# Kernel optimization log

Hardware: AMD Instinct MI355X
Metric: run time of the kernel (lower is better)

The kernel has to match this reference:

```python
import jax, jax.numpy as jnp
import numpy as np

V_SZ = 32000  # vocab_tar_size
D = 256       # embed / lstm / attn units
B, T, S = 32, 64, 128

def setup_inputs() -> dict:
    key = jax.random.key(0)
    ks = jax.random.split(key, 16)
    sc = lambda *shape: 1.0 / np.sqrt(shape[0])
    inp = {
        "tokens": jax.random.randint(ks[0], (B, T), 0, V_SZ),
        "h0": jax.random.normal(ks[1], (B, D), jnp.float32),
        "c0": jax.random.normal(ks[2], (B, D), jnp.float32),
        "enc_out": jax.random.normal(ks[3], (B, S, D), jnp.float32),
        # embedding table
        "E": jax.random.normal(ks[4], (V_SZ, D), jnp.float32) * 0.02,
        # attention: W1 (query), W2 (values/keys), V (score)
        "Wq": jax.random.normal(ks[5], (D, D), jnp.float32) * sc(D),
        "bq": jnp.zeros((D,), jnp.float32),
        "Wk": jax.random.normal(ks[6], (D, D), jnp.float32) * sc(D),
        "bk": jnp.zeros((D,), jnp.float32),
        "Vw": jax.random.normal(ks[7], (D, 1), jnp.float32) * sc(D),
        "bv": jnp.zeros((1,), jnp.float32),
        # LSTM: input dim 2D (context||embed), gates i,f,g,o
        "Wx": jax.random.normal(ks[8], (2 * D, 4 * D), jnp.float32) * sc(2 * D),
        "Wh": jax.random.normal(ks[9], (D, 4 * D), jnp.float32) * sc(D),
        "b_lstm": jnp.zeros((4 * D,), jnp.float32),
        # output projection + softmax
        "Wo": jax.random.normal(ks[10], (D, V_SZ), jnp.float32) * sc(D),
        "bo": jnp.zeros((V_SZ,), jnp.float32),
    }
    return inp


def reference(tokens, h0, c0, enc_out, E, Wq, bq, Wk, bk, Vw, bv,
              Wx, Wh, b_lstm, Wo, bo):
    # Precompute W2(values): same math as per-step recompute. [B,S,D]
    keys = enc_out @ Wk + bk

    def step(carry, tok):
        h, c = carry
        emb = E[tok]                                   # [B,D]
        # Bahdanau attention, query = h
        q = h @ Wq + bq                                # [B,D]
        score = jnp.tanh(q[:, None, :] + keys) @ Vw + bv   # [B,S,1]
        attn = jax.nn.softmax(score, axis=1)           # softmax over S
        ctx = jnp.sum(attn * enc_out, axis=1)          # [B,D]
        x = jnp.concatenate([ctx, emb], axis=-1)       # [B,2D]
        z = x @ Wx + h @ Wh + b_lstm                   # [B,4D]
        i, f, g, o = jnp.split(z, 4, axis=-1)          # keras gate order i,f,c,o
        c_new = jax.nn.sigmoid(f) * c + jax.nn.sigmoid(i) * jnp.tanh(g)
        h_new = jax.nn.sigmoid(o) * jnp.tanh(c_new)
        probs = jax.nn.softmax(h_new @ Wo + bo, axis=-1)   # [B,V]
        return (h_new, c_new), probs

    (_, _), outs = jax.lax.scan(step, (h0, c0), tokens.T)  # outs: [T,B,V]
    return jnp.transpose(outs, (1, 0, 2))                  # [B,T,V]
```

## Files before the change

kernel.cpp:

```cpp
#include <hip/hip_runtime.h>

#define Bz 32
#define Tz 64
#define Sz 128
#define Dz 256
#define Vz 32000

__device__ __forceinline__ float sigmf(float x){ return 1.0f/(1.0f + __expf(-x)); }
__device__ __forceinline__ float tanhfast(float x){ float e = __expf(2.0f*x); return 1.0f - 2.0f/(e+1.0f); }

__global__ void k_keys(const float* __restrict__ enc, const float* __restrict__ Wk,
                       const float* __restrict__ bk, float* __restrict__ keys){
  const int blk = blockIdx.x;
  const int tid = threadIdx.x;
  const int b  = blk >> 3;
  const int s0 = (blk & 7) * 16;
  const float* ebase = enc + (b*Sz + s0)*Dz;
  const int d = tid;
  float acc[16];
  #pragma unroll
  for (int i = 0; i < 16; ++i) acc[i] = 0.f;
  for (int k = 0; k < Dz; k += 4){
    float w0 = Wk[(k+0)*Dz + d];
    float w1 = Wk[(k+1)*Dz + d];
    float w2 = Wk[(k+2)*Dz + d];
    float w3 = Wk[(k+3)*Dz + d];
    #pragma unroll
    for (int si = 0; si < 16; ++si){
      float4 ev = *(const float4*)(ebase + si*Dz + k);
      acc[si] += ev.x*w0 + ev.y*w1 + ev.z*w2 + ev.w*w3;
    }
  }
  const float bkd = bk[d];
  #pragma unroll
  for (int si = 0; si < 16; ++si)
    keys[(b*Sz + s0 + si)*Dz + d] = acc[si] + bkd;
}

__global__ void __launch_bounds__(256) k_encw(const float* __restrict__ enc,
                                              const float* __restrict__ Wx,
                                              float* __restrict__ encW,
                                              unsigned* flags){
  const int tid = threadIdx.x;
  if (blockIdx.x == 0) flags[tid] = 0u;
  const int row0 = blockIdx.x * 4;
  const int u4 = tid * 4;
  float4 a0 = {0,0,0,0}, a1 = {0,0,0,0}, a2 = {0,0,0,0}, a3 = {0,0,0,0};
  for (int d = 0; d < Dz; ++d){
    float4 wv = *(const float4*)(Wx + (size_t)d*1024 + u4);
    float e0 = enc[(size_t)(row0+0)*Dz + d];
    float e1 = enc[(size_t)(row0+1)*Dz + d];
    float e2 = enc[(size_t)(row0+2)*Dz + d];
    float e3 = enc[(size_t)(row0+3)*Dz + d];
    a0.x += e0*wv.x; a0.y += e0*wv.y; a0.z += e0*wv.z; a0.w += e0*wv.w;
    a1.x += e1*wv.x; a1.y += e1*wv.y; a1.z += e1*wv.z; a1.w += e1*wv.w;
    a2.x += e2*wv.x; a2.y += e2*wv.y; a2.z += e2*wv.z; a2.w += e2*wv.w;
    a3.x += e3*wv.x; a3.y += e3*wv.y; a3.z += e3*wv.z; a3.w += e3*wv.w;
  }
  *(float4*)(encW + (size_t)(row0+0)*1024 + u4) = a0;
  *(float4*)(encW + (size_t)(row0+1)*1024 + u4) = a1;
  *(float4*)(encW + (size_t)(row0+2)*1024 + u4) = a2;
  *(float4*)(encW + (size_t)(row0+3)*1024 + u4) = a3;
}

__global__ void __launch_bounds__(1024) k_recur(
    const int* __restrict__ tok, const float* __restrict__ h0, const float* __restrict__ c0,
    const float* __restrict__ Emb,
    const float* __restrict__ Wq, const float* __restrict__ bq,
    const float* __restrict__ Vw, const float* __restrict__ bv,
    const float* __restrict__ Wx, const float* __restrict__ Wh,
    const float* __restrict__ bl, const float* __restrict__ keys,
    const float* __restrict__ encW,
    float* __restrict__ hs, float* xch, unsigned* flags)
{
  const int tid = threadIdx.x;
  const int blk = blockIdx.x;
  const int b = ((blk >> 6) << 3) | (blk & 7);
  const int s = (blk >> 3) & 7;

  __shared__ float ew[Sz*128];
  __shared__ float xe[512];
  __shared__ float qv[Dz];
  __shared__ float vl[Dz];
  __shared__ float scp[Sz];
  __shared__ float selds[Sz+1];
  __shared__ float zp[1024];
  __shared__ float zl[128];
  __shared__ float hnl[32];
  __shared__ float clds[32];
  __shared__ float qpp[1024];

  const int u_local = tid & 127;
  const int kc = tid >> 7;
  const int u_gate = ((u_local >> 5) << 8) + (s << 5) + (u_local & 31);
  const int dq = tid & 255;
  const int jc = tid >> 8;

  float w[64];
  {
    const float* wbase = (kc < 4) ? (Wx + (size_t)(256 + kc*64)*1024 + u_gate)
                                  : (Wh + (size_t)((kc-4)*64)*1024 + u_gate);
    #pragma unroll
    for (int i = 0; i < 64; ++i) w[i] = wbase[(size_t)i*1024];
  }
  float wq[8];
  #pragma unroll
  for (int jj = 0; jj < 8; ++jj) wq[jj] = Wq[(size_t)(s*32 + jc*8 + jj)*Dz + dq];

  #pragma unroll
  for (int i = 0; i < 16; ++i){
    int idx = tid + i*1024;
    int srow = idx >> 7, ul = idx & 127;
    int ug = ((ul >> 5) << 8) + (s << 5) + (ul & 31);
    ew[idx] = encW[(size_t)(b*Sz + srow)*1024 + ug];
  }

  if (tid < Dz) vl[tid] = Vw[tid];
  if (tid < 32) clds[tid] = c0[b*Dz + s*32 + tid];

  {
    float qp = 0.f;
    #pragma unroll
    for (int jj = 0; jj < 8; ++jj) qp += h0[b*Dz + s*32 + jc*8 + jj] * wq[jj];
    qpp[jc*256 + dq] = qp;
  }
  __syncthreads();
  {
    float* x0 = xch + (size_t)((b*8) + s)*288;
    if (tid < 256)
      __hip_atomic_store(x0 + tid, qpp[tid] + qpp[256+tid] + qpp[512+tid] + qpp[768+tid],
                         __ATOMIC_RELAXED, __HIP_MEMORY_SCOPE_AGENT);
    else if (tid < 288)
      __hip_atomic_store(x0 + tid, h0[b*Dz + s*32 + (tid-256)],
                         __ATOMIC_RELAXED, __HIP_MEMORY_SCOPE_AGENT);
  }
  __syncthreads();
  if (tid == 0)
    __hip_atomic_store(flags + b*8 + s, 1u, __ATOMIC_RELAXED, __HIP_MEMORY_SCOPE_AGENT);

  const float bv0 = bv[0];
  const int ss = tid >> 3, p8 = tid & 7;

  for (int t = 0; t < Tz; ++t){
    if (tid < 64){
      const unsigned tgt = (unsigned)(t+1);
      while (__hip_atomic_load(flags + b*8 + (tid & 7), __ATOMIC_RELAXED, __HIP_MEMORY_SCOPE_AGENT) < tgt)
        __builtin_amdgcn_s_sleep(1);
      __builtin_amdgcn_fence(__ATOMIC_ACQUIRE, "workgroup");
    }
    __syncthreads();
    const float* xcp = xch + (size_t)((t & 1)*256 + b*8)*288;
    if (tid < 256){
      float q = bq[tid];
      #pragma unroll
      for (int s2 = 0; s2 < 8; ++s2)
        q += __hip_atomic_load(xcp + s2*288 + tid, __ATOMIC_RELAXED, __HIP_MEMORY_SCOPE_AGENT);
      qv[tid] = q;
    } else if (tid < 512){
      int u = tid - 256;
      xe[256 + u] = __hip_atomic_load(xcp + (u >> 5)*288 + 256 + (u & 31),
                                      __ATOMIC_RELAXED, __HIP_MEMORY_SCOPE_AGENT);
    } else if (tid < 768){
      int eidx = tid - 512;
      int tk = tok[b*Tz + t];
      xe[eidx] = Emb[(size_t)tk*Dz + eidx];
    }
    __syncthreads();
    {
      const float* kp = keys + (size_t)(b*Sz + ss)*Dz;
      float a = 0.f;
      #pragma unroll
      for (int j4 = 0; j4 < 8; ++j4){
        const int d0 = j4*32 + p8*4;
        float4 kv = *(const float4*)(kp + d0);
        float4 qj = *(const float4*)(qv + d0);
        float4 vj = *(const float4*)(vl + d0);
        a += tanhfast(qj.x + kv.x) * vj.x;
        a += tanhfast(qj.y + kv.y) * vj.y;
        a += tanhfast(qj.z + kv.z) * vj.z;
        a += tanhfast(qj.w + kv.w) * vj.w;
      }
      a += __shfl_down(a, 4);
      a += __shfl_down(a, 2);
      a += __shfl_down(a, 1);
      if (p8 == 0) scp[ss] = a;
    }
    __syncthreads();
    if (tid < Sz) selds[tid] = __expf(scp[tid] + bv0);
    __syncthreads();
    if (tid < 64){
      float v = selds[tid] + selds[tid+64];
      #pragma unroll
      for (int off = 32; off > 0; off >>= 1) v += __shfl_down(v, off);
      if (tid == 0) selds[Sz] = 1.0f / v;
    }
    __syncthreads();
    {
      float acc1 = 0.f;
      const float* xep = xe + kc*64;
      #pragma unroll
      for (int i4 = 0; i4 < 16; ++i4){
        float4 xv = *(const float4*)(xep + i4*4);
        acc1 += xv.x*w[i4*4+0] + xv.y*w[i4*4+1] + xv.z*w[i4*4+2] + xv.w*w[i4*4+3];
      }
      float acc2 = 0.f;
      const float* ewp = ew + kc*16*128 + u_local;
      #pragma unroll
      for (int m = 0; m < 16; ++m)
        acc2 = __builtin_fmaf(selds[kc*16 + m], ewp[m*128], acc2);
      zp[kc*128 + u_local] = acc1 + selds[Sz]*acc2;
    }
    __syncthreads();
    if (tid < 128){
      float z = bl[((tid >> 5) << 8) + s*32 + (tid & 31)];
      #pragma unroll
      for (int k2 = 0; k2 < 8; ++k2) z += zp[k2*128 + tid];
      zl[tid] = z;
    }
    __syncthreads();
    if (tid < 32){
      float zi = zl[tid], zf = zl[32+tid], zg = zl[64+tid], zo = zl[96+tid];
      float cn = sigmf(zf)*clds[tid] + sigmf(zi)*tanhfast(zg);
      float hn = sigmf(zo)*tanhfast(cn);
      clds[tid] = cn; hnl[tid] = hn;
      hs[(size_t)(t*Bz + b)*Dz + s*32 + tid] = hn;
    }
    __syncthreads();
    if (t < Tz-1){
      {
        float qp = 0.f;
        #pragma unroll
        for (int jj = 0; jj < 8; ++jj) qp += hnl[jc*8 + jj] * wq[jj];
        qpp[jc*256 + dq] = qp;
      }
      __syncthreads();
      {
        float* xn = xch + (size_t)(((t+1) & 1)*256 + b*8 + s)*288;
        if (tid < 256)
          __hip_atomic_store(xn + tid, qpp[tid] + qpp[256+tid] + qpp[512+tid] + qpp[768+tid],
                             __ATOMIC_RELAXED, __HIP_MEMORY_SCOPE_AGENT);
        else if (tid < 288)
          __hip_atomic_store(xn + tid, hnl[tid - 256],
                             __ATOMIC_RELAXED, __HIP_MEMORY_SCOPE_AGENT);
      }
      __syncthreads();
      if (tid == 0)
        __hip_atomic_store(flags + b*8 + s, (unsigned)(t+2), __ATOMIC_RELAXED, __HIP_MEMORY_SCOPE_AGENT);
    }
  }
}

__global__ void __launch_bounds__(256) k_logits(
    const float* __restrict__ hs, const float* __restrict__ Wo, const float* __restrict__ bo,
    float* __restrict__ out, float* __restrict__ part)
{
  __shared__ float As[32][132];
  __shared__ float Bs[32][132];
  __shared__ float rs[128][17];
  const int tid = threadIdx.x;
  const int c0 = blockIdx.x * 128;
  const int R0 = blockIdx.y * 128;
  const int ty = tid >> 4;
  const int tx = tid & 15;
  float acc[8][8];
  #pragma unroll
  for (int i = 0; i < 8; ++i)
    #pragma unroll
    for (int j = 0; j < 8; ++j) acc[i][j] = 0.f;

  for (int k0 = 0; k0 < Dz; k0 += 32){
    #pragma unroll
    for (int i = 0; i < 4; ++i){
      int idx = tid + i*256;
      int r = idx >> 3, cq = idx & 7;
      float4 hv = *(const float4*)(hs + (size_t)(R0 + r)*Dz + k0 + cq*4);
      As[cq*4+0][r] = hv.x; As[cq*4+1][r] = hv.y; As[cq*4+2][r] = hv.z; As[cq*4+3][r] = hv.w;
    }
    #pragma unroll
    for (int i = 0; i < 4; ++i){
      int idx = tid + i*256;
      int kk = idx >> 5, c4 = idx & 31;
      float4 wv = *(const float4*)(Wo + (size_t)(k0 + kk)*Vz + c0 + c4*4);
      *(float4*)(&Bs[kk][c4*4]) = wv;
    }
    __syncthreads();
    #pragma unroll
    for (int kk = 0; kk < 32; ++kk){
      float4 a0 = *(const float4*)(&As[kk][ty*8]);
      float4 a1 = *(const float4*)(&As[kk][ty*8+4]);
      float a[8] = {a0.x,a0.y,a0.z,a0.w,a1.x,a1.y,a1.z,a1.w};
      float bb[8];
      #pragma unroll
      for (int j = 0; j < 8; ++j) bb[j] = Bs[kk][tx + 16*j];
      #pragma unroll
      for (int i = 0; i < 8; ++i)
        #pragma unroll
        for (int j = 0; j < 8; ++j)
          acc[i][j] = __builtin_fmaf(a[i], bb[j], acc[i][j]);
    }
    __syncthreads();
  }
  float rsum_loc[8];
  #pragma unroll
  for (int i = 0; i < 8; ++i) rsum_loc[i] = 0.f;
  #pragma unroll
  for (int i = 0; i < 8; ++i){
    const int R = R0 + ty*8 + i;
    const int orow = (R & 31)*64 + (R >> 5);
    float* orp = out + (size_t)orow*Vz + c0;
    #pragma unroll
    for (int j = 0; j < 8; ++j){
      const int col = tx + 16*j;
      float p = __expf(acc[i][j] + bo[c0 + col]);
      orp[col] = p;
      rsum_loc[i] += p;
    }
  }
  #pragma unroll
  for (int i = 0; i < 8; ++i) rs[ty*8+i][tx] = rsum_loc[i];
  __syncthreads();
  if (tid < 128){
    float ssum = 0.f;
    #pragma unroll
    for (int x = 0; x < 16; ++x) ssum += rs[tid][x];
    part[(size_t)blockIdx.x*2048 + R0 + tid] = ssum;
  }
}

__global__ void __launch_bounds__(256) k_scale(float* __restrict__ out, const float* __restrict__ part){
  const int row = blockIdx.x;
  const int b = row >> 6, tt = row & 63;
  const int R = tt*Bz + b;
  const int tid = threadIdx.x;
  __shared__ float ssum[4];
  float v = (tid < 250) ? part[(size_t)tid*2048 + R] : 0.f;
  #pragma unroll
  for (int off = 32; off > 0; off >>= 1) v += __shfl_down(v, off);
  if ((tid & 63) == 0) ssum[tid >> 6] = v;
  __syncthreads();
  const float inv = 1.0f / (ssum[0] + ssum[1] + ssum[2] + ssum[3]);
  float4* rp = (float4*)(out + (size_t)row*Vz);
  for (int j4 = tid; j4 < Vz/4; j4 += 256){
    float4 x = rp[j4];
    x.x *= inv; x.y *= inv; x.z *= inv; x.w *= inv;
    rp[j4] = x;
  }
}

extern "C" void kernel_launch(void* const* d_in, const int* in_sizes, int n_in,
                              void* d_out, int out_size, void* d_ws, size_t ws_size,
                              hipStream_t stream){
  const int*   tok = (const int*)  d_in[0];
  const float* h0  = (const float*)d_in[1];
  const float* c0  = (const float*)d_in[2];
  const float* enc = (const float*)d_in[3];
  const float* E   = (const float*)d_in[4];
  const float* Wq  = (const float*)d_in[5];
  const float* bq  = (const float*)d_in[6];
  const float* Wk  = (const float*)d_in[7];
  const float* bk  = (const float*)d_in[8];
  const float* Vw  = (const float*)d_in[9];
  const float* bv  = (const float*)d_in[10];
  const float* Wx  = (const float*)d_in[11];
  const float* Wh  = (const float*)d_in[12];
  const float* bl  = (const float*)d_in[13];
  const float* Wo  = (const float*)d_in[14];
  const float* bo  = (const float*)d_in[15];
  float* out = (float*)d_out;
  float* ws  = (float*)d_ws;

  float* keys = ws;
  float* encW = keys + 1048576;
  float* hs   = encW + 4194304;
  float* xchg = hs   + 524288;
  unsigned* flags = (unsigned*)(xchg + 147456);
  float* part = encW;

  hipLaunchKernelGGL(k_keys, dim3(256), dim3(256), 0, stream, enc, Wk, bk, keys);
  hipLaunchKernelGGL(k_encw, dim3(1024), dim3(256), 0, stream, enc, Wx, encW, flags);
  hipLaunchKernelGGL(k_recur, dim3(256), dim3(1024), 0, stream,
                     tok, h0, c0, E, Wq, bq, Vw, bv, Wx, Wh, bl, keys, encW,
                     hs, xchg, flags);
  hipLaunchKernelGGL(k_logits, dim3(250,16), dim3(256), 0, stream, hs, Wo, bo, out, part);
  hipLaunchKernelGGL(k_scale, dim3(2048), dim3(256), 0, stream, out, part);
}
```

Baseline: 1.479 ms.

## Fuse recurrence and logits into a persistent kernel with flag-driven overlap

Merges the encW precompute, the LSTM recurrence and the vocabulary projection into one 506-block kernel. The first 256 blocks compute their encW slice locally and run the recurrence, while 250 extra blocks spin on per-batch step flags and compute logits for each completed group of four timesteps. This overlaps the output GEMM with the serial recurrence and drops the encW global round-trip and two launches. It relies on all 506 blocks being co-resident to avoid deadlock, and the logits tile shrinks to 4x4 per thread, which may lower GEMM efficiency.

```diff
diff --git a/kernel.cpp b/kernel.cpp
--- a/kernel.cpp
+++ b/kernel.cpp
@@ -10,9 +10,11 @@
 __device__ __forceinline__ float tanhfast(float x){ float e = __expf(2.0f*x); return 1.0f - 2.0f/(e+1.0f); }
 
 __global__ void k_keys(const float* __restrict__ enc, const float* __restrict__ Wk,
-                       const float* __restrict__ bk, float* __restrict__ keys){
+                       const float* __restrict__ bk, float* __restrict__ keys,
+                       unsigned* __restrict__ flags){
   const int blk = blockIdx.x;
   const int tid = threadIdx.x;
+  if (blk == 0) flags[tid] = 0u;
   const int b  = blk >> 3;
   const int s0 = (blk & 7) * 16;
   const float* ebase = enc + (b*Sz + s0)*Dz;
@@ -37,293 +39,279 @@
     keys[(b*Sz + s0 + si)*Dz + d] = acc[si] + bkd;
 }
 
-__global__ void __launch_bounds__(256) k_encw(const float* __restrict__ enc,
-                                              const float* __restrict__ Wx,
-                                              float* __restrict__ encW,
-                                              unsigned* flags){
-  const int tid = threadIdx.x;
-  if (blockIdx.x == 0) flags[tid] = 0u;
-  const int row0 = blockIdx.x * 4;
-  const int u4 = tid * 4;
-  float4 a0 = {0,0,0,0}, a1 = {0,0,0,0}, a2 = {0,0,0,0}, a3 = {0,0,0,0};
-  for (int d = 0; d < Dz; ++d){
-    float4 wv = *(const float4*)(Wx + (size_t)d*1024 + u4);
-    float e0 = enc[(size_t)(row0+0)*Dz + d];
-    float e1 = enc[(size_t)(row0+1)*Dz + d];
-    float e2 = enc[(size_t)(row0+2)*Dz + d];
-    float e3 = enc[(size_t)(row0+3)*Dz + d];
-    a0.x += e0*wv.x; a0.y += e0*wv.y; a0.z += e0*wv.z; a0.w += e0*wv.w;
-    a1.x += e1*wv.x; a1.y += e1*wv.y; a1.z += e1*wv.z; a1.w += e1*wv.w;
-    a2.x += e2*wv.x; a2.y += e2*wv.y; a2.z += e2*wv.z; a2.w += e2*wv.w;
-    a3.x += e3*wv.x; a3.y += e3*wv.y; a3.z += e3*wv.z; a3.w += e3*wv.w;
-  }
-  *(float4*)(encW + (size_t)(row0+0)*1024 + u4) = a0;
-  *(float4*)(encW + (size_t)(row0+1)*1024 + u4) = a1;
-  *(float4*)(encW + (size_t)(row0+2)*1024 + u4) = a2;
-  *(float4*)(encW + (size_t)(row0+3)*1024 + u4) = a3;
-}
-
-__global__ void __launch_bounds__(1024) k_recur(
+__global__ void __launch_bounds__(1024, 8) k_mega(
     const int* __restrict__ tok, const float* __restrict__ h0, const float* __restrict__ c0,
-    const float* __restrict__ Emb,
+    const float* __restrict__ enc, const float* __restrict__ Emb,
     const float* __restrict__ Wq, const float* __restrict__ bq,
     const float* __restrict__ Vw, const float* __restrict__ bv,
     const float* __restrict__ Wx, const float* __restrict__ Wh,
-    const float* __restrict__ bl, const float* __restrict__ keys,
-    const float* __restrict__ encW,
-    float* __restrict__ hs, float* xch, unsigned* flags)
+    const float* __restrict__ bl, const float* __restrict__ Wo,
+    const float* __restrict__ bo, const float* __restrict__ keys,
+    float* __restrict__ hs, float* xch, unsigned* flags,
+    float* __restrict__ out, float* __restrict__ part)
 {
+  __shared__ float smem[18628];
   const int tid = threadIdx.x;
-  const int blk = blockIdx.x;
-  const int b = ((blk >> 6) << 3) | (blk & 7);
-  const int s = (blk >> 3) & 7;
-
-  __shared__ float ew[Sz*128];
-  __shared__ float xe[512];
-  __shared__ float qv[Dz];
-  __shared__ float vl[Dz];
-  __shared__ float scp[Sz];
-  __shared__ float selds[Sz+1];
-  __shared__ float zp[1024];
-  __shared__ float zl[128];
-  __shared__ float hnl[32];
-  __shared__ float clds[32];
-  __shared__ float qpp[1024];
-
-  const int u_local = tid & 127;
-  const int kc = tid >> 7;
-  const int u_gate = ((u_local >> 5) << 8) + (s << 5) + (u_local & 31);
-  const int dq = tid & 255;
-  const int jc = tid >> 8;
-
-  float w[64];
-  {
-    const float* wbase = (kc < 4) ? (Wx + (size_t)(256 + kc*64)*1024 + u_gate)
-                                  : (Wh + (size_t)((kc-4)*64)*1024 + u_gate);
+
+  if (blockIdx.x < 256){
+    const int blk = blockIdx.x;
+    const int b = ((blk >> 6) << 3) | (blk & 7);
+    const int s = (blk >> 3) & 7;
+
+    float* ew    = smem;
+    float* xe    = ew + 16384;
+    float* qv    = xe + 512;
+    float* vl    = qv + 256;
+    float* selds = vl + 256;
+    float* zp    = selds + 132;
+    float* hnl   = zp + 1024;
+    float* clds  = hnl + 32;
+
+    const int u_local = tid & 127;
+    const int kc = tid >> 7;
+    const int u_gate = ((u_local >> 5) << 8) + (s << 5) + (u_local & 31);
+
+    {
+      float acc[16];
+      #pragma unroll
+      for (int i = 0; i < 16; ++i) acc[i] = 0.f;
+      const float* eb = enc + (size_t)(b*Sz + kc*16)*Dz;
+      for (int d4 = 0; d4 < Dz; d4 += 4){
+        float w0 = Wx[(size_t)(d4+0)*1024 + u_gate];
+        float w1 = Wx[(size_t)(d4+1)*1024 + u_gate];
+        float w2 = Wx[(size_t)(d4+2)*1024 + u_gate];
+        float w3 = Wx[(size_t)(d4+3)*1024 + u_gate];
+        #pragma unroll
+        for (int i = 0; i < 16; ++i){
+          float4 ev = *(const float4*)(eb + (size_t)i*Dz + d4);
+          acc[i] += ev.x*w0 + ev.y*w1 + ev.z*w2 + ev.w*w3;
+        }
+      }
+      #pragma unroll
+      for (int i = 0; i < 16; ++i) ew[(kc*16 + i)*128 + u_local] = acc[i];
+    }
+
+    float w[64];
+    {
+      const float* wbase = (kc < 4) ? (Wx + (size_t)(256 + kc*64)*1024 + u_gate)
+                                    : (Wh + (size_t)((kc-4)*64)*1024 + u_gate);
+      #pragma unroll
+      for (int i = 0; i < 64; ++i) w[i] = wbase[(size_t)i*1024];
+    }
+    const int dq = tid & 255;
+    float wq[32];
     #pragma unroll
-    for (int i = 0; i < 64; ++i) w[i] = wbase[(size_t)i*1024];
-  }
-  float wq[8];
-  #pragma unroll
-  for (int jj = 0; jj < 8; ++jj) wq[jj] = Wq[(size_t)(s*32 + jc*8 + jj)*Dz + dq];
-
-  #pragma unroll
-  for (int i = 0; i < 16; ++i){
-    int idx = tid + i*1024;
-    int srow = idx >> 7, ul = idx & 127;
-    int ug = ((ul >> 5) << 8) + (s << 5) + (ul & 31);
-    ew[idx] = encW[(size_t)(b*Sz + srow)*1024 + ug];
-  }
-
-  if (tid < Dz) vl[tid] = Vw[tid];
-  if (tid < 32) clds[tid] = c0[b*Dz + s*32 + tid];
-
-  {
-    float qp = 0.f;
-    #pragma unroll
-    for (int jj = 0; jj < 8; ++jj) qp += h0[b*Dz + s*32 + jc*8 + jj] * wq[jj];
-    qpp[jc*256 + dq] = qp;
-  }
-  __syncthreads();
-  {
-    float* x0 = xch + (size_t)((b*8) + s)*288;
-    if (tid < 256)
-      __hip_atomic_store(x0 + tid, qpp[tid] + qpp[256+tid] + qpp[512+tid] + qpp[768+tid],
-                         __ATOMIC_RELAXED, __HIP_MEMORY_SCOPE_AGENT);
-    else if (tid < 288)
-      __hip_atomic_store(x0 + tid, h0[b*Dz + s*32 + (tid-256)],
-                         __ATOMIC_RELAXED, __HIP_MEMORY_SCOPE_AGENT);
-  }
-  __syncthreads();
-  if (tid == 0)
-    __hip_atomic_store(flags + b*8 + s, 1u, __ATOMIC_RELAXED, __HIP_MEMORY_SCOPE_AGENT);
-
-  const float bv0 = bv[0];
-  const int ss = tid >> 3, p8 = tid & 7;
-
-  for (int t = 0; t < Tz; ++t){
-    if (tid < 64){
-      const unsigned tgt = (unsigned)(t+1);
-      while (__hip_atomic_load(flags + b*8 + (tid & 7), __ATOMIC_RELAXED, __HIP_MEMORY_SCOPE_AGENT) < tgt)
-        __builtin_amdgcn_s_sleep(1);
+    for (int u = 0; u < 32; ++u) wq[u] = Wq[(size_t)(s*32 + u)*Dz + dq];
+
+    if (tid < Dz) vl[tid] = Vw[tid];
+    if (tid < 32){ hnl[tid] = h0[b*Dz + s*32 + tid]; clds[tid] = c0[b*Dz + s*32 + tid]; }
+    __syncthreads();
+
+    {
+      float* xn = xch + (size_t)(b*8 + s)*288;
+      if (tid < 256){
+        float qp = 0.f;
+        #pragma unroll
+        for (int u = 0; u < 32; ++u) qp = __builtin_fmaf(hnl[u], wq[u], qp);
+        __hip_atomic_store(xn + tid, qp, __ATOMIC_RELAXED, __HIP_MEMORY_SCOPE_AGENT);
+      } else if (tid < 288){
+        __hip_atomic_store(xn + tid, hnl[tid - 256], __ATOMIC_RELAXED, __HIP_MEMORY_SCOPE_AGENT);
+      } else if (tid >= 512 && tid < 768){
+        const int tk = tok[b*Tz + 0];
+        xe[tid - 512] = Emb[(size_t)tk*Dz + (tid - 512)];
+      }
+      __syncthreads();
+      if (tid == 0)
+        __hip_atomic_store(flags + b*8 + s, 1u, __ATOMIC_RELAXED, __HIP_MEMORY_SCOPE_AGENT);
+    }
+
+    const float bv0 = bv[0];
+    const int ss = tid >> 3, p8 = tid & 7;
+
+    for (int t = 0; t < Tz; ++t){
+      if (tid < 8){
+        const unsigned tgt = (unsigned)(t + 1);
+        while (__hip_atomic_load(flags + b*8 + tid, __ATOMIC_RELAXED, __HIP_MEMORY_SCOPE_AGENT) < tgt)
+          __builtin_amdgcn_s_sleep(1);
+      }
+      __syncthreads();
       __builtin_amdgcn_fence(__ATOMIC_ACQUIRE, "workgroup");
-    }
-    __syncthreads();
-    const float* xcp = xch + (size_t)((t & 1)*256 + b*8)*288;
-    if (tid < 256){
-      float q = bq[tid];
-      #pragma unroll
-      for (int s2 = 0; s2 < 8; ++s2)
-        q += __hip_atomic_load(xcp + s2*288 + tid, __ATOMIC_RELAXED, __HIP_MEMORY_SCOPE_AGENT);
-      qv[tid] = q;
-    } else if (tid < 512){
-      int u = tid - 256;
-      xe[256 + u] = __hip_atomic_load(xcp + (u >> 5)*288 + 256 + (u & 31),
-                                      __ATOMIC_RELAXED, __HIP_MEMORY_SCOPE_AGENT);
-    } else if (tid < 768){
-      int eidx = tid - 512;
-      int tk = tok[b*Tz + t];
-      xe[eidx] = Emb[(size_t)tk*Dz + eidx];
-    }
-    __syncthreads();
-    {
-      const float* kp = keys + (size_t)(b*Sz + ss)*Dz;
-      float a = 0.f;
-      #pragma unroll
-      for (int j4 = 0; j4 < 8; ++j4){
-        const int d0 = j4*32 + p8*4;
-        float4 kv = *(const float4*)(kp + d0);
-        float4 qj = *(const float4*)(qv + d0);
-        float4 vj = *(const float4*)(vl + d0);
-        a += tanhfast(qj.x + kv.x) * vj.x;
-        a += tanhfast(qj.y + kv.y) * vj.y;
-        a += tanhfast(qj.z + kv.z) * vj.z;
-        a += tanhfast(qj.w + kv.w) * vj.w;
-      }
-      a += __shfl_down(a, 4);
-      a += __shfl_down(a, 2);
-      a += __shfl_down(a, 1);
-      if (p8 == 0) scp[ss] = a;
-    }
-    __syncthreads();
-    if (tid < Sz) selds[tid] = __expf(scp[tid] + bv0);
-    __syncthreads();
-    if (tid < 64){
-      float v = selds[tid] + selds[tid+64];
-      #pragma unroll
-      for (int off = 32; off > 0; off >>= 1) v += __shfl_down(v, off);
-      if (tid == 0) selds[Sz] = 1.0f / v;
-    }
-    __syncthreads();
-    {
-      float acc1 = 0.f;
-      const float* xep = xe + kc*64;
-      #pragma unroll
-      for (int i4 = 0; i4 < 16; ++i4){
-        float4 xv = *(const float4*)(xep + i4*4);
-        acc1 += xv.x*w[i4*4+0] + xv.y*w[i4*4+1] + xv.z*w[i4*4+2] + xv.w*w[i4*4+3];
-      }
-      float acc2 = 0.f;
-      const float* ewp = ew + kc*16*128 + u_local;
-      #pragma unroll
-      for (int m = 0; m < 16; ++m)
-        acc2 = __builtin_fmaf(selds[kc*16 + m], ewp[m*128], acc2);
-      zp[kc*128 + u_local] = acc1 + selds[Sz]*acc2;
-    }
-    __syncthreads();
-    if (tid < 128){
-      float z = bl[((tid >> 5) << 8) + s*32 + (tid & 31)];
-      #pragma unroll
-      for (int k2 = 0; k2 < 8; ++k2) z += zp[k2*128 + tid];
-      zl[tid] = z;
-    }
-    __syncthreads();
-    if (tid < 32){
-      float zi = zl[tid], zf = zl[32+tid], zg = zl[64+tid], zo = zl[96+tid];
-      float cn = sigmf(zf)*clds[tid] + sigmf(zi)*tanhfast(zg);
-      float hn = sigmf(zo)*tanhfast(cn);
-      clds[tid] = cn; hnl[tid] = hn;
-      hs[(size_t)(t*Bz + b)*Dz + s*32 + tid] = hn;
-    }
-    __syncthreads();
-    if (t < Tz-1){
+
+      const float* xcp = xch + (size_t)((t & 1)*256 + b*8)*288;
+      if (tid < 256){
+        float q = bq[tid];
+        #pragma unroll
+        for (int s2 = 0; s2 < 8; ++s2)
+          q += __hip_atomic_load(xcp + s2*288 + tid, __ATOMIC_RELAXED, __HIP_MEMORY_SCOPE_AGENT);
+        qv[tid] = q;
+      } else if (tid < 512){
+        const int u = tid - 256;
+        xe[256 + u] = __hip_atomic_load(xcp + (u >> 5)*288 + 256 + (u & 31),
+                                        __ATOMIC_RELAXED, __HIP_MEMORY_SCOPE_AGENT);
+      }
+      __syncthreads();
       {
-        float qp = 0.f;
-        #pragma unroll
-        for (int jj = 0; jj < 8; ++jj) qp += hnl[jc*8 + jj] * wq[jj];
-        qpp[jc*256 + dq] = qp;
+        const float* kp = keys + (size_t)(b*Sz + ss)*Dz;
+        float a = 0.f;
+        #pragma unroll
+        for (int j4 = 0; j4 < 8; ++j4){
+          const int d0 = j4*32 + p8*4;
+          float4 kv = *(const float4*)(kp + d0);
+          float4 qj = *(const float4*)(qv + d0);
+          float4 vj = *(const float4*)(vl + d0);
+          a += tanhfast(qj.x + kv.x) * vj.x;
+          a += tanhfast(qj.y + kv.y) * vj.y;
+          a += tanhfast(qj.z + kv.z) * vj.z;
+          a += tanhfast(qj.w + kv.w) * vj.w;
+        }
+        a += __shfl_down(a, 4);
+        a += __shfl_down(a, 2);
+        a += __shfl_down(a, 1);
+        if (p8 == 0) selds[ss] = __expf(a + bv0);
+      }
+      __syncthreads();
+      if (tid < 64){
+        float v = selds[tid] + selds[tid + 64];
+        #pragma unroll
+        for (int off = 32; off > 0; off >>= 1) v += __shfl_down(v, off);
+        if (tid == 0) selds[Sz] = 1.0f / v;
+      }
+      __syncthreads();
+      {
+        float acc1 = 0.f;
+        const float* xep = xe + kc*64;
+        #pragma unroll
+        for (int i4 = 0; i4 < 16; ++i4){
+          float4 xv = *(const float4*)(xep + i4*4);
+          acc1 += xv.x*w[i4*4+0] + xv.y*w[i4*4+1] + xv.z*w[i4*4+2] + xv.w*w[i4*4+3];
+        }
+        float acc2 = 0.f;
+        const float* ewp = ew + kc*16*128 + u_local;
+        #pragma unroll
+        for (int m = 0; m < 16; ++m)
+          acc2 = __builtin_fmaf(selds[kc*16 + m], ewp[m*128], acc2);
+        zp[kc*128 + u_local] = acc1 + selds[Sz]*acc2;
+      }
+      __syncthreads();
+      if (tid < 32){
+        const int u = tid;
+        float zi = bl[         s*32 + u], zf = bl[  Dz + s*32 + u];
+        float zg = bl[2*Dz + s*32 + u], zo = bl[3*Dz + s*32 + u];
+        #pragma unroll
+        for (int k2 = 0; k2 < 8; ++k2){
+          zi += zp[k2*128 +      u];
+          zf += zp[k2*128 + 32 + u];
+          zg += zp[k2*128 + 64 + u];
+          zo += zp[k2*128 + 96 + u];
+        }
+        float cn = sigmf(zf)*clds[u] + sigmf(zi)*tanhfast(zg);
+        float hn = sigmf(zo)*tanhfast(cn);
+        clds[u] = cn; hnl[u] = hn;
+        __hip_atomic_store(hs + (size_t)(t*Bz + b)*Dz + s*32 + u, hn,
+                           __ATOMIC_RELAXED, __HIP_MEMORY_SCOPE_AGENT);
       }
       __syncthreads();
       {
         float* xn = xch + (size_t)(((t+1) & 1)*256 + b*8 + s)*288;
+        if (tid < 256){
+          float qp = 0.f;
+          #pragma unroll
+          for (int u = 0; u < 32; ++u) qp = __builtin_fmaf(hnl[u], wq[u], qp);
+          __hip_atomic_store(xn + tid, qp, __ATOMIC_RELAXED, __HIP_MEMORY_SCOPE_AGENT);
+        } else if (tid < 288){
+          __hip_atomic_store(xn + tid, hnl[tid - 256], __ATOMIC_RELAXED, __HIP_MEMORY_SCOPE_AGENT);
+        } else if (tid >= 512 && tid < 768 && t+1 < Tz){
+          const int tk = tok[b*Tz + t + 1];
+          xe[tid - 512] = Emb[(size_t)tk*Dz + (tid - 512)];
+        }
+        __syncthreads();
+        if (tid == 0)
+          __hip_atomic_store(flags + b*8 + s, (unsigned)(t + 2), __ATOMIC_RELAXED, __HIP_MEMORY_SCOPE_AGENT);
+      }
+    }
+  } else {
+    const int wid = blockIdx.x - 256;
+    float* As = smem;
+    float* Bs = As + 32*132;
+    float* rs = Bs + 32*132;
+
+    const int ty = tid >> 5;
+    const int tx = tid & 31;
+    const int c0 = wid * 128;
+
+    for (int y = 0; y < 16; ++y){
+      const unsigned tgt = (unsigned)(4*y + 5);
+      for (;;){
+        int ok = 1;
         if (tid < 256)
-          __hip_atomic_store(xn + tid, qpp[tid] + qpp[256+tid] + qpp[512+tid] + qpp[768+tid],
-                             __ATOMIC_RELAXED, __HIP_MEMORY_SCOPE_AGENT);
-        else if (tid < 288)
-          __hip_atomic_store(xn + tid, hnl[tid - 256],
-                             __ATOMIC_RELAXED, __HIP_MEMORY_SCOPE_AGENT);
-      }
-      __syncthreads();
-      if (tid == 0)
-        __hip_atomic_store(flags + b*8 + s, (unsigned)(t+2), __ATOMIC_RELAXED, __HIP_MEMORY_SCOPE_AGENT);
-    }
-  }
-}
-
-__global__ void __launch_bounds__(256) k_logits(
-    const float* __restrict__ hs, const float* __restrict__ Wo, const float* __restrict__ bo,
-    float* __restrict__ out, float* __restrict__ part)
-{
-  __shared__ float As[32][132];
-  __shared__ float Bs[32][132];
-  __shared__ float rs[128][17];
-  const int tid = threadIdx.x;
-  const int c0 = blockIdx.x * 128;
-  const int R0 = blockIdx.y * 128;
-  const int ty = tid >> 4;
-  const int tx = tid & 15;
-  float acc[8][8];
-  #pragma unroll
-  for (int i = 0; i < 8; ++i)
-    #pragma unroll
-    for (int j = 0; j < 8; ++j) acc[i][j] = 0.f;
-
-  for (int k0 = 0; k0 < Dz; k0 += 32){
-    #pragma unroll
-    for (int i = 0; i < 4; ++i){
-      int idx = tid + i*256;
-      int r = idx >> 3, cq = idx & 7;
-      float4 hv = *(const float4*)(hs + (size_t)(R0 + r)*Dz + k0 + cq*4);
-      As[cq*4+0][r] = hv.x; As[cq*4+1][r] = hv.y; As[cq*4+2][r] = hv.z; As[cq*4+3][r] = hv.w;
-    }
-    #pragma unroll
-    for (int i = 0; i < 4; ++i){
-      int idx = tid + i*256;
-      int kk = idx >> 5, c4 = idx & 31;
-      float4 wv = *(const float4*)(Wo + (size_t)(k0 + kk)*Vz + c0 + c4*4);
-      *(float4*)(&Bs[kk][c4*4]) = wv;
-    }
-    __syncthreads();
-    #pragma unroll
-    for (int kk = 0; kk < 32; ++kk){
-      float4 a0 = *(const float4*)(&As[kk][ty*8]);
-      float4 a1 = *(const float4*)(&As[kk][ty*8+4]);
-      float a[8] = {a0.x,a0.y,a0.z,a0.w,a1.x,a1.y,a1.z,a1.w};
-      float bb[8];
-      #pragma unroll
-      for (int j = 0; j < 8; ++j) bb[j] = Bs[kk][tx + 16*j];
-      #pragma unroll
-      for (int i = 0; i < 8; ++i)
-        #pragma unroll
-        for (int j = 0; j < 8; ++j)
-          acc[i][j] = __builtin_fmaf(a[i], bb[j], acc[i][j]);
-    }
-    __syncthreads();
-  }
-  float rsum_loc[8];
-  #pragma unroll
-  for (int i = 0; i < 8; ++i) rsum_loc[i] = 0.f;
-  #pragma unroll
-  for (int i = 0; i < 8; ++i){
-    const int R = R0 + ty*8 + i;
-    const int orow = (R & 31)*64 + (R >> 5);
-    float* orp = out + (size_t)orow*Vz + c0;
-    #pragma unroll
-    for (int j = 0; j < 8; ++j){
-      const int col = tx + 16*j;
-      float p = __expf(acc[i][j] + bo[c0 + col]);
-      orp[col] = p;
-      rsum_loc[i] += p;
-    }
-  }
-  #pragma unroll
-  for (int i = 0; i < 8; ++i) rs[ty*8+i][tx] = rsum_loc[i];
-  __syncthreads();
-  if (tid < 128){
-    float ssum = 0.f;
-    #pragma unroll
-    for (int x = 0; x < 16; ++x) ssum += rs[tid][x];
-    part[(size_t)blockIdx.x*2048 + R0 + tid] = ssum;
+          ok = (__hip_atomic_load(flags + tid, __ATOMIC_RELAXED, __HIP_MEMORY_SCOPE_AGENT) >= tgt);
+        if (__syncthreads_count(ok) == 1024) break;
+        __builtin_amdgcn_s_sleep(16);
+      }
+      __builtin_amdgcn_fence(__ATOMIC_ACQUIRE, "workgroup");
+
+      const int R0 = y * 128;
+      float acc[4][4];
+      #pragma unroll
+      for (int i = 0; i < 4; ++i)
+        #pragma unroll
+        for (int j = 0; j < 4; ++j) acc[i][j] = 0.f;
+
+      for (int k0 = 0; k0 < Dz; k0 += 32){
+        {
+          const int r = tid >> 3, kq = tid & 7;
+          const float* hp = hs + (size_t)(R0 + r)*Dz + k0 + kq*4;
+          float a0 = __hip_atomic_load(hp+0, __ATOMIC_RELAXED, __HIP_MEMORY_SCOPE_AGENT);
+          float a1 = __hip_atomic_load(hp+1, __ATOMIC_RELAXED, __HIP_MEMORY_SCOPE_AGENT);
+          float a2 = __hip_atomic_load(hp+2, __ATOMIC_RELAXED, __HIP_MEMORY_SCOPE_AGENT);
+          float a3 = __hip_atomic_load(hp+3, __ATOMIC_RELAXED, __HIP_MEMORY_SCOPE_AGENT);
+          As[(kq*4+0)*132 + r] = a0;
+          As[(kq*4+1)*132 + r] = a1;
+          As[(kq*4+2)*132 + r] = a2;
+          As[(kq*4+3)*132 + r] = a3;
+        }
+        {
+          const int kk = tid >> 5, c4 = tid & 31;
+          float4 wv = *(const float4*)(Wo + (size_t)(k0 + kk)*Vz + c0 + c4*4);
+          *(float4*)(Bs + kk*132 + c4*4) = wv;
+        }
+        __syncthreads();
+        #pragma unroll
+        for (int kk = 0; kk < 32; ++kk){
+          float4 av  = *(const float4*)(As + kk*132 + ty*4);
+          float4 bv4 = *(const float4*)(Bs + kk*132 + tx*4);
+          float ar[4] = {av.x, av.y, av.z, av.w};
+          float br[4] = {bv4.x, bv4.y, bv4.z, bv4.w};
+          #pragma unroll
+          for (int i = 0; i < 4; ++i)
+            #pragma unroll
+            for (int j = 0; j < 4; ++j)
+              acc[i][j] = __builtin_fmaf(ar[i], br[j], acc[i][j]);
+        }
+        __syncthreads();
+      }
+      float4 bo4 = *(const float4*)(bo + c0 + tx*4);
+      #pragma unroll
+      for (int i = 0; i < 4; ++i){
+        const int R = R0 + ty*4 + i;
+        const int orow = (R & 31)*64 + (R >> 5);
+        float4 pv;
+        pv.x = __expf(acc[i][0] + bo4.x);
+        pv.y = __expf(acc[i][1] + bo4.y);
+        pv.z = __expf(acc[i][2] + bo4.z);
+        pv.w = __expf(acc[i][3] + bo4.w);
+        *(float4*)(out + (size_t)orow*Vz + c0 + tx*4) = pv;
+        rs[(ty*4+i)*33 + tx] = pv.x + pv.y + pv.z + pv.w;
+      }
+      __syncthreads();
+      if (tid < 128){
+        float ssum = 0.f;
+        #pragma unroll
+        for (int x = 0; x < 32; ++x) ssum += rs[tid*33 + x];
+        part[(size_t)wid*2048 + R0 + tid] = ssum;
+      }
+      __syncthreads();
+    }
   }
 }
 
@@ -370,17 +358,14 @@
   float* ws  = (float*)d_ws;
 
   float* keys = ws;
-  float* encW = keys + 1048576;
-  float* hs   = encW + 4194304;
-  float* xchg = hs   + 524288;
-  unsigned* flags = (unsigned*)(xchg + 147456);
-  float* part = encW;
-
-  hipLaunchKernelGGL(k_keys, dim3(256), dim3(256), 0, stream, enc, Wk, bk, keys);
-  hipLaunchKernelGGL(k_encw, dim3(1024), dim3(256), 0, stream, enc, Wx, encW, flags);
-  hipLaunchKernelGGL(k_recur, dim3(256), dim3(1024), 0, stream,
-                     tok, h0, c0, E, Wq, bq, Vw, bv, Wx, Wh, bl, keys, encW,
-                     hs, xchg, flags);
-  hipLaunchKernelGGL(k_logits, dim3(250,16), dim3(256), 0, stream, hs, Wo, bo, out, part);
+  float* hs   = keys + 1048576;
+  float* xch  = hs   + 524288;
+  float* part = xch  + 147456;
+  unsigned* flags = (unsigned*)(part + 512000);
+
+  hipLaunchKernelGGL(k_keys, dim3(256), dim3(256), 0, stream, enc, Wk, bk, keys, flags);
+  hipLaunchKernelGGL(k_mega, dim3(506), dim3(1024), 0, stream,
+                     tok, h0, c0, enc, E, Wq, bq, Vw, bv, Wx, Wh, bl, Wo, bo,
+                     keys, hs, xch, flags, out, part);
   hipLaunchKernelGGL(k_scale, dim3(2048), dim3(256), 0, stream, out, part);
 }
```

New measurement: 3.051 ms. 2.06x slower.
